# Performance work log

Hardware: AMD Instinct MI355X
Metric: run time of the kernel (lower is better)

The kernel has to match this reference:

```python
import jax, jax.numpy as jnp
import numpy as np

N, FIN, F, H = 4096, 128, 64, 8
NEG = -1e10


def setup_inputs() -> dict:
    key = jax.random.key(0)
    ks = jax.random.split(key, 6)
    X = jax.random.normal(ks[0], (N, FIN), dtype=jnp.float32)
    # sparse-ish binary adjacency with self loops, stored dense (as the layer expects)
    A = (jax.random.uniform(ks[1], (N, N)) < 0.05).astype(jnp.int32)
    A = A.at[jnp.arange(N), jnp.arange(N)].set(1)
    W = jax.random.normal(ks[2], (H, FIN, F), dtype=jnp.float32) * (1.0 / np.sqrt(FIN))
    b = jnp.zeros((H, F), dtype=jnp.float32)
    a_self = jax.random.normal(ks[3], (H, F), dtype=jnp.float32) * (1.0 / np.sqrt(F))
    a_neigh = jax.random.normal(ks[4], (H, F), dtype=jnp.float32) * (1.0 / np.sqrt(F))
    return {"X": X, "A": A, "W": W, "b": b, "a_self": a_self, "a_neigh": a_neigh}


def reference(X, A, W, b, a_self, a_neigh):
    # Dropout layers run in inference mode in the original call -> identity.
    feats = jnp.einsum('nf,hfo->hno', X, W)              # [H, N, F]
    s_self = jnp.einsum('hno,ho->hn', feats, a_self)     # [H, N]
    s_neigh = jnp.einsum('hno,ho->hn', feats, a_neigh)   # [H, N]
    scores = s_self[:, :, None] + s_neigh[:, None, :]    # [H, N, N]
    scores = jnp.where(scores > 0, scores, 0.2 * scores)  # LeakyReLU(0.2)
    mask = (1.0 - A.astype(jnp.float32)) * NEG            # [N, N]
    attn = jax.nn.softmax(scores + mask[None], axis=-1)   # [H, N, N]
    out = jnp.einsum('hnm,hmo->hno', attn, feats) + b[:, None, :]
    out = jax.nn.elu(out)                                 # [H, N, F]
    # concat heads -> [N, H*F]
    return jnp.transpose(out, (1, 0, 2)).reshape(N, H * F)
```

## Files before the change

### kernel.cpp

```cpp
#include <hip/hip_runtime.h>
#include <cmath>


#define NN 4096
#define FIN 128
#define FF 64
#define HH 8

typedef _Float16 h2 __attribute__((ext_vector_type(2)));
typedef _Float16 h4 __attribute__((ext_vector_type(4)));
typedef _Float16 h8 __attribute__((ext_vector_type(8)));
typedef float f32x2 __attribute__((ext_vector_type(2)));
typedef float f32x4 __attribute__((ext_vector_type(4)));

union H8 {
  h8 v;
  h2 p[4];
};
union U2 {
  h2 h;
  unsigned u;
};

static __device__ __forceinline__ unsigned mask2(unsigned w, int j) {
#if __has_builtin(__builtin_amdgcn_sbfe) && __has_builtin(__builtin_amdgcn_perm)
  int lo = __builtin_amdgcn_sbfe((int)w, j, 1);
  int hi = __builtin_amdgcn_sbfe((int)w, j + 1, 1);
  return __builtin_amdgcn_perm((unsigned)hi, (unsigned)lo, 0x05040100u);
#else
  int lo = ((int)(w << (31 - j))) >> 31;
  int hi = ((int)(w << (30 - j))) >> 31;
  return ((unsigned)lo & 0xFFFFu) | ((unsigned)hi << 16);
#endif
}

static __device__ __forceinline__ void gload16(const void* g, void* l) {
  __builtin_amdgcn_global_load_lds(
      (const __attribute__((address_space(1))) unsigned int*)g,
      (__attribute__((address_space(3))) unsigned int*)l, 16, 0, 0);
}

__global__ __launch_bounds__(256) void pack_kernel(
    const int* __restrict__ A, const float* __restrict__ W,
    const float* __restrict__ X, unsigned long long* __restrict__ bits,
    _Float16* __restrict__ Wsw, _Float16* __restrict__ Xsw) {
  const int b = blockIdx.x;
  const int tid = threadIdx.x;
  const int wave = tid >> 6, lane = tid & 63;
  if (b < NN) {
    __shared__ int ldsT[4][4][256];
    const int* ar = A + (size_t)b * NN;
    int4 v[4];
#pragma unroll
    for (int it = 0; it < 4; ++it) {
      const int g = wave * 4 + it;
      v[it] = *(const int4*)(ar + g * 256 + lane * 4);
    }
#pragma unroll
    for (int it = 0; it < 4; ++it) *(int4*)&ldsT[wave][it][lane * 4] = v[it];
    unsigned long long* br = bits + ((size_t)b << 6);
#pragma unroll
    for (int it = 0; it < 4; ++it) {
      const int g = wave * 4 + it;
      int w0 = ldsT[wave][it][0 * 64 + lane];
      int w1 = ldsT[wave][it][1 * 64 + lane];
      int w2 = ldsT[wave][it][2 * 64 + lane];
      int w3 = ldsT[wave][it][3 * 64 + lane];
      unsigned long long m0 = __ballot(w0 != 0);
      unsigned long long m1 = __ballot(w1 != 0);
      unsigned long long m2 = __ballot(w2 != 0);
      unsigned long long m3 = __ballot(w3 != 0);
      if (lane == 0) {
        ulonglong2 p0 = {m0, m1}, p1 = {m2, m3};
        *(ulonglong2*)(br + g * 4 + 0) = p0;
        *(ulonglong2*)(br + g * 4 + 2) = p1;
      }
    }
  } else if (b < NN + 2) {
    const int h0 = (b - NN) * 4;
    for (int h = h0; h < h0 + 4; ++h) {
      for (int c = tid; c < 1024; c += 256) {
        int ln = c & 63, nb = (c >> 6) & 3, kt = c >> 8;
        int f = nb * 16 + (ln & 15);
        int k0 = kt * 32 + (ln >> 4) * 8;
        h8 v;
#pragma unroll
        for (int j = 0; j < 8; ++j)
          v[j] = (_Float16)W[((size_t)(h * FIN) + k0 + j) * FF + f];
        *(h8*)(Wsw + ((size_t)(((h * 4 + kt) * 4 + nb) * 64 + ln)) * 8) = v;
      }
    }
  } else {
    const int tile = (b - NN - 2) * 4 + wave;
    const int l16 = lane & 15, quad = lane >> 4;
    const float* xr = X + (size_t)(tile * 16 + l16) * FIN;
#pragma unroll
    for (int kt = 0; kt < 4; ++kt) {
      int k0 = kt * 32 + quad * 8;
      f32x4 x0 = *(const f32x4*)(xr + k0);
      f32x4 x1 = *(const f32x4*)(xr + k0 + 4);
      h8 v = {(_Float16)x0[0], (_Float16)x0[1], (_Float16)x0[2],
              (_Float16)x0[3], (_Float16)x1[0], (_Float16)x1[1],
              (_Float16)x1[2], (_Float16)x1[3]};
      *(h8*)(Xsw + ((size_t)((tile * 4 + kt) * 64 + lane)) * 8) = v;
    }
  }
}

__global__ __launch_bounds__(256) void feats_kernel(
    const _Float16* __restrict__ Xsw, const _Float16* __restrict__ Wsw,
    const float* __restrict__ a_self, const float* __restrict__ a_neigh,
    _Float16* __restrict__ feats_sw, _Float16* __restrict__ es_h,
    _Float16* __restrict__ esn_h, _Float16* __restrict__ et_h,
    _Float16* __restrict__ etn_h) {
  const int h = blockIdx.y;
  const int tid = threadIdx.x, wave = tid >> 6, lane = tid & 63;
  const int l16 = lane & 15, quad = lane >> 4;
  const int rt = blockIdx.x * 4 + wave;
  const int r0 = rt * 16;

  f32x4 acc[4];
#pragma unroll
  for (int nb = 0; nb < 4; ++nb) acc[nb] = (f32x4){0.f, 0.f, 0.f, 0.f};

  const _Float16* xp = Xsw + ((size_t)(rt * 4) * 64 + lane) * 8;
  const _Float16* wp = Wsw + ((size_t)(h * 16) * 64 + lane) * 8;
  h8 Af[4];
#pragma unroll
  for (int kt = 0; kt < 4; ++kt) Af[kt] = *(const h8*)(xp + kt * 512);
#pragma unroll
  for (int kt = 0; kt < 4; ++kt)
#pragma unroll
    for (int nb = 0; nb < 4; ++nb) {
      h8 Bf = *(const h8*)(wp + (kt * 4 + nb) * 512);
      acc[nb] = __builtin_amdgcn_mfma_f32_16x16x32_f16(Af[kt], Bf, acc[nb], 0, 0, 0);
    }

  float as[4], an[4];
#pragma unroll
  for (int nb = 0; nb < 4; ++nb) {
    as[nb] = a_self[h * FF + nb * 16 + l16];
    an[nb] = a_neigh[h * FF + nb * 16 + l16];
  }
#pragma unroll
  for (int r = 0; r < 4; ++r) {
    float ps = acc[0][r] * as[0] + acc[1][r] * as[1] + acc[2][r] * as[2] +
               acc[3][r] * as[3];
    float pn = acc[0][r] * an[0] + acc[1][r] * an[1] + acc[2][r] * an[2] +
               acc[3][r] * an[3];
#pragma unroll
    for (int m = 1; m <= 8; m <<= 1) {
      ps += __shfl_xor(ps, m, 64);
      pn += __shfl_xor(pn, m, 64);
    }
    if (l16 == 0) {
      int node = h * NN + r0 + quad * 4 + r;
      es_h[node] = (_Float16)__expf(ps - 2.0f);
      esn_h[node] = (_Float16)__expf(0.2f * ps - 2.0f);
      et_h[node] = (_Float16)__expf(pn - 2.0f);
      etn_h[node] = (_Float16)__expf(0.2f * pn - 2.0f);
    }
  }

  const int kb = r0 >> 5;
  const int quadA = ((r0 >> 4) & 1) * 2 + (quad >> 1);
  const int jbase = (quad & 1) << 2;
#pragma unroll
  for (int nb = 0; nb < 4; ++nb) {
    h4 v = {(_Float16)acc[nb][0], (_Float16)acc[nb][1], (_Float16)acc[nb][2],
            (_Float16)acc[nb][3]};
    size_t off = ((size_t)((h * 128 + kb) * 4 + nb) << 9) +
                 ((quadA * 16 + l16) << 3) + jbase;
    *(h4*)(feats_sw + off) = v;
  }
}

__global__ __launch_bounds__(512, 4) void attn_kernel(
    const unsigned long long* __restrict__ Abits,
    const _Float16* __restrict__ feats_sw, const _Float16* __restrict__ es_h,
    const _Float16* __restrict__ esn_h, const _Float16* __restrict__ et_h,
    const _Float16* __restrict__ etn_h, const float* __restrict__ bias,
    float* __restrict__ out) {
  const int bid = blockIdx.x;
  const int h = bid & 7, n0 = (bid >> 3) << 6;
  const int tid = threadIdx.x, wave = tid >> 6, lane = tid & 63;
  const int l16 = lane & 15, quad = lane >> 4;
  const int shq = quad << 3;
  const int rh = wave & 1, ctw = (wave >> 1) & 1, kfw = wave >> 2;

  __shared__ __align__(16) char smem[3 * 19456];

  h2 esp[2], esnp[2];
#pragma unroll
  for (int rt = 0; rt < 2; ++rt) {
    const int myrow = n0 + (rh << 5) + (rt << 4) + l16;
    _Float16 e = es_h[h * NN + myrow];
    _Float16 en = esn_h[h * NN + myrow];
    esp[rt] = (h2){e, e};
    esnp[rt] = (h2){en, en};
  }

  f32x4 acc[2][4], accd[2];
#pragma unroll
  for (int rt = 0; rt < 2; ++rt) {
    accd[rt] = (f32x4){0.f, 0.f, 0.f, 0.f};
#pragma unroll
    for (int nb = 0; nb < 4; ++nb) acc[rt][nb] = (f32x4){0.f, 0.f, 0.f, 0.f};
  }
  const h8 ONES = {(_Float16)1.f, (_Float16)1.f, (_Float16)1.f, (_Float16)1.f,
                   (_Float16)1.f, (_Float16)1.f, (_Float16)1.f, (_Float16)1.f};

  const char* gF = (const char*)feats_sw + ((size_t)h << 19);
  const char* gE = (const char*)et_h + (h << 13);
  const char* gEN = (const char*)etn_h + (h << 13);
  const char* gB = (const char*)Abits + ((size_t)n0 << 9);

#define STAGE(s_, bw_)                                                         \
  do {                                                                         \
    char* L_ = smem + (bw_)*19456;                                             \
    const char* src_ = gF + ((size_t)(s_) << 14) + (wave << 11) + (lane << 4); \
    gload16(src_, L_ + (wave << 11) + (lane << 4));                            \
    gload16(src_ + 1024, L_ + (wave << 11) + 1024 + (lane << 4));              \
    if (wave == 0)                                                             \
      gload16(gE + ((s_) << 8) + (l16 << 4), L_ + 16384 + (lane << 4));        \
    if (wave == 1)                                                             \
      gload16(gEN + ((s_) << 8) + (l16 << 4), L_ + 17408 + (lane << 4));       \
    if (wave == 2)                                                             \
      gload16(gB + ((size_t)lane << 9) + ((s_) << 4), L_ + 18432 + (lane << 4)); \
  } while (0)

  STAGE(0, 0);
  STAGE(1, 1);

  for (int s = 0; s < 32; ++s) {
    __builtin_amdgcn_sched_barrier(0);
    if (s < 31) {
      if (wave < 3)
        asm volatile("s_waitcnt vmcnt(3)" ::: "memory");
      else
        asm volatile("s_waitcnt vmcnt(2)" ::: "memory");
    } else {
      asm volatile("s_waitcnt vmcnt(0)" ::: "memory");
    }
    __builtin_amdgcn_sched_barrier(0);
    __builtin_amdgcn_s_barrier();
    if (s < 30) STAGE(s + 2, (s + 2) % 3);

    const char* L = smem + (s % 3) * 19456;
    unsigned long long mb0 = *(const unsigned long long*)(
        L + 18432 + (((rh << 5) + l16) << 4) + (ctw << 3));
    unsigned long long mb1 = *(const unsigned long long*)(
        L + 18432 + (((rh << 5) + 16 + l16) << 4) + (ctw << 3));
    H8 ET, ETN;
    ET.v = *(const h8*)(L + 16384 + (ctw << 7) + (kfw << 6) + (quad << 4));
    ETN.v = *(const h8*)(L + 17408 + (ctw << 7) + (kfw << 6) + (quad << 4));
    const char* fB = L + (ctw << 13) + (kfw << 12) + (lane << 4);
    h8 B0 = *(const h8*)(fB);
    h8 B1 = *(const h8*)(fB + 1024);
    h8 B2 = *(const h8*)(fB + 2048);
    h8 B3 = *(const h8*)(fB + 3072);

#pragma unroll
    for (int rt = 0; rt < 2; ++rt) {
      unsigned long long myb = rt ? mb1 : mb0;
      unsigned wsw = (unsigned)(myb >> (kfw ? 32 : 0)) >> shq;
      H8 P;
#pragma unroll
      for (int p = 0; p < 4; ++p) {
        h2 a_ = esp[rt] * ET.p[p];
        h2 b_ = esnp[rt] * ETN.p[p];
        h2 r_ = __builtin_elementwise_max(a_, b_);
        U2 u_;
        u_.h = r_;
        u_.u &= mask2(wsw, 2 * p);
        P.p[p] = u_.h;
      }
      acc[rt][0] =
          __builtin_amdgcn_mfma_f32_16x16x32_f16(P.v, B0, acc[rt][0], 0, 0, 0);
      acc[rt][1] =
          __builtin_amdgcn_mfma_f32_16x16x32_f16(P.v, B1, acc[rt][1], 0, 0, 0);
      acc[rt][2] =
          __builtin_amdgcn_mfma_f32_16x16x32_f16(P.v, B2, acc[rt][2], 0, 0, 0);
      acc[rt][3] =
          __builtin_amdgcn_mfma_f32_16x16x32_f16(P.v, B3, acc[rt][3], 0, 0, 0);
      accd[rt] =
          __builtin_amdgcn_mfma_f32_16x16x32_f16(P.v, ONES, accd[rt], 0, 0, 0);
    }
  }
#undef STAGE

  float(*accL)[16][68] = (float(*)[16][68])smem;
  float* denL = (float*)(smem + 8 * 16 * 68 * 4);
  const int erow = tid >> 4;
  const int rh_o = erow >> 4, r16 = erow & 15;
  const int ec0 = (tid & 15) << 2;
#pragma unroll
  for (int rt = 0; rt < 2; ++rt) {
    __syncthreads();
#pragma unroll
    for (int nb = 0; nb < 4; ++nb)
#pragma unroll
      for (int r = 0; r < 4; ++r)
        accL[wave][quad * 4 + r][nb * 16 + l16] = acc[rt][nb][r];
    if (l16 == 0) {
#pragma unroll
      for (int r = 0; r < 4; ++r) denL[wave * 16 + quad * 4 + r] = accd[rt][r];
    }
    __syncthreads();
    f32x4 v = (f32x4){0.f, 0.f, 0.f, 0.f};
    float dn = 0.f;
#pragma unroll
    for (int cw = 0; cw < 4; ++cw) {
      const int w = rh_o + ((cw & 1) << 1) + ((cw >> 1) << 2);
      v += *(const f32x4*)&accL[w][r16][ec0];
      dn += denL[w * 16 + r16];
    }
    float inv = 1.0f / dn;
    const f32x4 bv = *(const f32x4*)(bias + h * FF + ec0);
#pragma unroll
    for (int i = 0; i < 4; ++i) {
      float x = v[i] * inv + bv[i];
      v[i] = x > 0.f ? x : (__expf(x) - 1.0f);
    }
    *(f32x4*)(out + (size_t)(n0 + (rh_o << 5) + (rt << 4) + r16) * (HH * FF) +
              h * FF + ec0) = v;
  }
}

extern "C" void kernel_launch(void* const* d_in, const int* in_sizes, int n_in,
                              void* d_out, int out_size, void* d_ws,
                              size_t ws_size, hipStream_t stream) {
  const float* X = (const float*)d_in[0];
  const int* A = (const int*)d_in[1];
  const float* W = (const float*)d_in[2];
  const float* b = (const float*)d_in[3];
  const float* a_self = (const float*)d_in[4];
  const float* a_neigh = (const float*)d_in[5];
  float* out = (float*)d_out;

  char* ws = (char*)d_ws;
  unsigned long long* Abits = (unsigned long long*)ws;
  _Float16* feats_sw = (_Float16*)(ws + (2u << 20));
  _Float16* es_h = (_Float16*)(ws + (6u << 20));
  _Float16* esn_h = (_Float16*)(ws + (6u << 20) + (64u << 10));
  _Float16* et_h = (_Float16*)(ws + (6u << 20) + (128u << 10));
  _Float16* etn_h = (_Float16*)(ws + (6u << 20) + (192u << 10));
  _Float16* Wsw = (_Float16*)(ws + (6u << 20) + (256u << 10));
  _Float16* Xsw = (_Float16*)(ws + (6u << 20) + (384u << 10));

  pack_kernel<<<NN + 66, 256, 0, stream>>>(A, W, X, Abits, Wsw, Xsw);
  feats_kernel<<<dim3(64, 8), 256, 0, stream>>>(Xsw, Wsw, a_self, a_neigh,
                                                feats_sw, es_h, esn_h, et_h,
                                                etn_h);
  attn_kernel<<<512, 512, 0, stream>>>(Abits, feats_sw, es_h, esn_h, et_h,
                                       etn_h, b, out);
}
```

Baseline: 143.9 us.

## Restructure attention kernel to 4 waves with larger K tiles and double buffering

The attention kernel goes from 8 waves to 4 waves per block. Each wave now covers all 64 rows with 4 row tiles, so every B fragment loaded from LDS feeds 4 row tiles instead of 2. Each stage now loads a 256-column K tile (16 iterations instead of 32), and the pipeline changes from triple buffering with partial vmcnt waits to double buffering with a full vmcnt(0) wait. The epilogue reduces across the 4 waves in a single pass. The intent is to cut per-stage barrier count and LDS reads per MFMA, at the cost of more accumulator registers, lower occupancy, and less latency hiding from the shallower prefetch.

Result: slower. 148.9 us (+3.5%).

```diff
diff --git a/kernel.cpp b/kernel.cpp
--- a/kernel.cpp
+++ b/kernel.cpp
@@ -175,7 +175,7 @@
   }
 }
 
-__global__ __launch_bounds__(512, 4) void attn_kernel(
+__global__ __launch_bounds__(256, 2) void attn_kernel(
     const unsigned long long* __restrict__ Abits,
     const _Float16* __restrict__ feats_sw, const _Float16* __restrict__ es_h,
     const _Float16* __restrict__ esn_h, const _Float16* __restrict__ et_h,
@@ -186,23 +186,23 @@
   const int tid = threadIdx.x, wave = tid >> 6, lane = tid & 63;
   const int l16 = lane & 15, quad = lane >> 4;
   const int shq = quad << 3;
-  const int rh = wave & 1, ctw = (wave >> 1) & 1, kfw = wave >> 2;
-
-  __shared__ __align__(16) char smem[3 * 19456];
-
-  h2 esp[2], esnp[2];
-#pragma unroll
-  for (int rt = 0; rt < 2; ++rt) {
-    const int myrow = n0 + (rh << 5) + (rt << 4) + l16;
+  const int ctw = wave & 1, kfw = wave >> 1;
+
+  __shared__ __align__(16) char smem[2 * 36864];
+
+  h2 esp[4], esnp[4];
+#pragma unroll
+  for (int rt = 0; rt < 4; ++rt) {
+    const int myrow = n0 + (rt << 4) + l16;
     _Float16 e = es_h[h * NN + myrow];
     _Float16 en = esn_h[h * NN + myrow];
     esp[rt] = (h2){e, e};
     esnp[rt] = (h2){en, en};
   }
 
-  f32x4 acc[2][4], accd[2];
-#pragma unroll
-  for (int rt = 0; rt < 2; ++rt) {
+  f32x4 acc[4][4], accd[4];
+#pragma unroll
+  for (int rt = 0; rt < 4; ++rt) {
     accd[rt] = (f32x4){0.f, 0.f, 0.f, 0.f};
 #pragma unroll
     for (int nb = 0; nb < 4; ++nb) acc[rt][nb] = (f32x4){0.f, 0.f, 0.f, 0.f};
@@ -215,115 +215,119 @@
   const char* gEN = (const char*)etn_h + (h << 13);
   const char* gB = (const char*)Abits + ((size_t)n0 << 9);
 
-#define STAGE(s_, bw_)                                                         \
+  const unsigned fO = (wave << 13) + (lane << 4);
+  const unsigned eO = lane << 4;
+  const unsigned bO = ((lane >> 1) << 9) + ((lane & 1) << 4);
+
+#define STAGE(s_, L_)                                                          \
   do {                                                                         \
-    char* L_ = smem + (bw_)*19456;                                             \
-    const char* src_ = gF + ((size_t)(s_) << 14) + (wave << 11) + (lane << 4); \
-    gload16(src_, L_ + (wave << 11) + (lane << 4));                            \
-    gload16(src_ + 1024, L_ + (wave << 11) + 1024 + (lane << 4));              \
+    const char* sf_ = gF + ((size_t)(s_) << 15) + fO;                          \
+    _Pragma("unroll") for (int i = 0; i < 8; ++i)                              \
+        gload16(sf_ + (i << 10), (L_) + fO + (i << 10));                       \
     if (wave == 0)                                                             \
-      gload16(gE + ((s_) << 8) + (l16 << 4), L_ + 16384 + (lane << 4));        \
+      gload16(gE + ((s_) << 9) + eO, (L_) + 32768 + eO);                       \
     if (wave == 1)                                                             \
-      gload16(gEN + ((s_) << 8) + (l16 << 4), L_ + 17408 + (lane << 4));       \
+      gload16(gEN + ((s_) << 9) + eO, (L_) + 33792 + eO);                      \
     if (wave == 2)                                                             \
-      gload16(gB + ((size_t)lane << 9) + ((s_) << 4), L_ + 18432 + (lane << 4)); \
+      gload16(gB + bO + ((s_) << 5), (L_) + 34816 + eO);                       \
+    if (wave == 3)                                                             \
+      gload16(gB + 16384 + bO + ((s_) << 5), (L_) + 35840 + eO);               \
   } while (0)
 
-  STAGE(0, 0);
-  STAGE(1, 1);
-
-  for (int s = 0; s < 32; ++s) {
+  STAGE(0, smem);
+
+  const unsigned etOff = 32768 + (ctw << 8) + (kfw << 6) + (quad << 4);
+  const unsigned fbOff = (ctw << 14) + (kfw << 12) + (lane << 4);
+  const unsigned btOff = 34816 + (l16 << 5) + (ctw << 4);
+
+  for (int s = 0; s < 16; ++s) {
+    char* L = smem + (s & 1) * 36864;
+    char* Ln = smem + ((s + 1) & 1) * 36864;
     __builtin_amdgcn_sched_barrier(0);
-    if (s < 31) {
-      if (wave < 3)
-        asm volatile("s_waitcnt vmcnt(3)" ::: "memory");
-      else
-        asm volatile("s_waitcnt vmcnt(2)" ::: "memory");
-    } else {
-      asm volatile("s_waitcnt vmcnt(0)" ::: "memory");
-    }
+    asm volatile("s_waitcnt vmcnt(0)" ::: "memory");
     __builtin_amdgcn_sched_barrier(0);
     __builtin_amdgcn_s_barrier();
-    if (s < 30) STAGE(s + 2, (s + 2) % 3);
-
-    const char* L = smem + (s % 3) * 19456;
-    unsigned long long mb0 = *(const unsigned long long*)(
-        L + 18432 + (((rh << 5) + l16) << 4) + (ctw << 3));
-    unsigned long long mb1 = *(const unsigned long long*)(
-        L + 18432 + (((rh << 5) + 16 + l16) << 4) + (ctw << 3));
-    H8 ET, ETN;
-    ET.v = *(const h8*)(L + 16384 + (ctw << 7) + (kfw << 6) + (quad << 4));
-    ETN.v = *(const h8*)(L + 17408 + (ctw << 7) + (kfw << 6) + (quad << 4));
-    const char* fB = L + (ctw << 13) + (kfw << 12) + (lane << 4);
-    h8 B0 = *(const h8*)(fB);
-    h8 B1 = *(const h8*)(fB + 1024);
-    h8 B2 = *(const h8*)(fB + 2048);
-    h8 B3 = *(const h8*)(fB + 3072);
-
-#pragma unroll
-    for (int rt = 0; rt < 2; ++rt) {
-      unsigned long long myb = rt ? mb1 : mb0;
-      unsigned wsw = (unsigned)(myb >> (kfw ? 32 : 0)) >> shq;
-      H8 P;
-#pragma unroll
-      for (int p = 0; p < 4; ++p) {
-        h2 a_ = esp[rt] * ET.p[p];
-        h2 b_ = esnp[rt] * ETN.p[p];
-        h2 r_ = __builtin_elementwise_max(a_, b_);
-        U2 u_;
-        u_.h = r_;
-        u_.u &= mask2(wsw, 2 * p);
-        P.p[p] = u_.h;
+    if (s < 15) STAGE(s + 1, Ln);
+
+#pragma unroll
+    for (int ctp = 0; ctp < 2; ++ctp) {
+      H8 ET, ETN;
+      ET.v = *(const h8*)(L + etOff + (ctp << 7));
+      ETN.v = *(const h8*)(L + 1024 + etOff + (ctp << 7));
+      const char* fB = L + fbOff + (ctp << 13);
+      h8 B0 = *(const h8*)(fB);
+      h8 B1 = *(const h8*)(fB + 1024);
+      h8 B2 = *(const h8*)(fB + 2048);
+      h8 B3 = *(const h8*)(fB + 3072);
+#pragma unroll
+      for (int rt = 0; rt < 4; ++rt) {
+        unsigned long long myb = *(const unsigned long long*)(
+            L + btOff + (rt << 9) + (ctp << 3));
+        unsigned wsw = (unsigned)(myb >> (kfw ? 32 : 0)) >> shq;
+        H8 P;
+#pragma unroll
+        for (int p = 0; p < 4; ++p) {
+          h2 a_ = esp[rt] * ET.p[p];
+          h2 b_ = esnp[rt] * ETN.p[p];
+          h2 r_ = __builtin_elementwise_max(a_, b_);
+          U2 u_;
+          u_.h = r_;
+          u_.u &= mask2(wsw, 2 * p);
+          P.p[p] = u_.h;
+        }
+        acc[rt][0] = __builtin_amdgcn_mfma_f32_16x16x32_f16(P.v, B0,
+                                                            acc[rt][0], 0, 0, 0);
+        acc[rt][1] = __builtin_amdgcn_mfma_f32_16x16x32_f16(P.v, B1,
+                                                            acc[rt][1], 0, 0, 0);
+        acc[rt][2] = __builtin_amdgcn_mfma_f32_16x16x32_f16(P.v, B2,
+                                                            acc[rt][2], 0, 0, 0);
+        acc[rt][3] = __builtin_amdgcn_mfma_f32_16x16x32_f16(P.v, B3,
+                                                            acc[rt][3], 0, 0, 0);
+        accd[rt] = __builtin_amdgcn_mfma_f32_16x16x32_f16(P.v, ONES, accd[rt],
+                                                          0, 0, 0);
       }
-      acc[rt][0] =
-          __builtin_amdgcn_mfma_f32_16x16x32_f16(P.v, B0, acc[rt][0], 0, 0, 0);
-      acc[rt][1] =
-          __builtin_amdgcn_mfma_f32_16x16x32_f16(P.v, B1, acc[rt][1], 0, 0, 0);
-      acc[rt][2] =
-          __builtin_amdgcn_mfma_f32_16x16x32_f16(P.v, B2, acc[rt][2], 0, 0, 0);
-      acc[rt][3] =
-          __builtin_amdgcn_mfma_f32_16x16x32_f16(P.v, B3, acc[rt][3], 0, 0, 0);
-      accd[rt] =
-          __builtin_amdgcn_mfma_f32_16x16x32_f16(P.v, ONES, accd[rt], 0, 0, 0);
     }
   }
 #undef STAGE
 
-  float(*accL)[16][68] = (float(*)[16][68])smem;
-  float* denL = (float*)(smem + 8 * 16 * 68 * 4);
-  const int erow = tid >> 4;
-  const int rh_o = erow >> 4, r16 = erow & 15;
+  float(*accL)[64][68] = (float(*)[64][68])smem;
+  float* denL = (float*)(smem + 4 * 64 * 68 * 4);
+  __syncthreads();
+#pragma unroll
+  for (int rt = 0; rt < 4; ++rt) {
+#pragma unroll
+    for (int nb = 0; nb < 4; ++nb)
+#pragma unroll
+      for (int r = 0; r < 4; ++r)
+        accL[wave][(rt << 4) + (quad << 2) + r][(nb << 4) + l16] =
+            acc[rt][nb][r];
+    if (l16 == 0) {
+#pragma unroll
+      for (int r = 0; r < 4; ++r)
+        denL[(wave << 6) + (rt << 4) + (quad << 2) + r] = accd[rt][r];
+    }
+  }
+  __syncthreads();
   const int ec0 = (tid & 15) << 2;
-#pragma unroll
-  for (int rt = 0; rt < 2; ++rt) {
-    __syncthreads();
-#pragma unroll
-    for (int nb = 0; nb < 4; ++nb)
-#pragma unroll
-      for (int r = 0; r < 4; ++r)
-        accL[wave][quad * 4 + r][nb * 16 + l16] = acc[rt][nb][r];
-    if (l16 == 0) {
-#pragma unroll
-      for (int r = 0; r < 4; ++r) denL[wave * 16 + quad * 4 + r] = accd[rt][r];
-    }
-    __syncthreads();
+  const f32x4 bv = *(const f32x4*)(bias + h * FF + ec0);
+#pragma unroll
+  for (int k = 0; k < 4; ++k) {
+    const int row = (tid >> 4) + (k << 4);
     f32x4 v = (f32x4){0.f, 0.f, 0.f, 0.f};
     float dn = 0.f;
 #pragma unroll
-    for (int cw = 0; cw < 4; ++cw) {
-      const int w = rh_o + ((cw & 1) << 1) + ((cw >> 1) << 2);
-      v += *(const f32x4*)&accL[w][r16][ec0];
-      dn += denL[w * 16 + r16];
+    for (int w = 0; w < 4; ++w) {
+      v += *(const f32x4*)&accL[w][row][ec0];
+      dn += denL[(w << 6) + row];
     }
     float inv = 1.0f / dn;
-    const f32x4 bv = *(const f32x4*)(bias + h * FF + ec0);
+    f32x4 o;
 #pragma unroll
     for (int i = 0; i < 4; ++i) {
       float x = v[i] * inv + bv[i];
-      v[i] = x > 0.f ? x : (__expf(x) - 1.0f);
-    }
-    *(f32x4*)(out + (size_t)(n0 + (rh_o << 5) + (rt << 4) + r16) * (HH * FF) +
-              h * FF + ec0) = v;
+      o[i] = x > 0.f ? x : (__expf(x) - 1.0f);
+    }
+    *(f32x4*)(out + (size_t)(n0 + row) * (HH * FF) + h * FF + ec0) = o;
   }
 }
 
@@ -352,6 +356,6 @@
   feats_kernel<<<dim3(64, 8), 256, 0, stream>>>(Xsw, Wsw, a_self, a_neigh,
                                                 feats_sw, es_h, esn_h, et_h,
                                                 etn_h);
-  attn_kernel<<<512, 512, 0, stream>>>(Abits, feats_sw, es_h, esn_h, et_h,
+  attn_kernel<<<512, 256, 0, stream>>>(Abits, feats_sw, es_h, esn_h, et_h,
                                        etn_h, b, out);
 }
```
